# Performance work log

Measured on AMD Instinct MI355X. Metric: run time of the kernel, lower is better.

The kernel has to match this reference:

```python
import jax, jax.numpy as jnp
import numpy as np

N = 50000   # nodes per graph
E = 400000  # edges per graph (avg degree 8)
L = 16      # regex token length per edge
V = 64      # VOCAB_SIZE
EMB = 32    # REGEX_EMBEDDING_DIMENSION
H = 128     # LSTM_DIMENSION
D = 373     # hidden_vector_dim (MAX_STATES=50)
IN_IDX = 161
OUT_IDX = 320
SID = 53    # MAX_STATES + 3
SLOPE = 0.2 # GATv2 leaky_relu negative slope

def _lstm_cell(x_t, h, c, Wih, Whh, b):
    g = x_t @ Wih.T + h @ Whh.T + b          # [E, 4H], torch gate order i,f,g,o
    i, f, gg, o = jnp.split(g, 4, axis=-1)
    c = jax.nn.sigmoid(f) * c + jax.nn.sigmoid(i) * jnp.tanh(gg)
    h = jax.nn.sigmoid(o) * jnp.tanh(c)
    return h, c

def _edge_scalar(tokens, embed, Wih_f, Whh_f, b_f, Wih_r, Whh_r, b_r, W1, b1, W2, b2):
    emb = embed.at[0].set(0.0)[tokens]       # padding_idx=0; [E, L, EMB]
    En = tokens.shape[0]
    h0 = jnp.zeros((En, H), jnp.float32)
    def step(carry, x_t):
        h, c = _lstm_cell(x_t, carry[0], carry[1], Wih_f, Whh_f, b_f)
        return (h, c), None
    (h_fwd, _), _ = jax.lax.scan(step, (h0, h0), jnp.swapaxes(emb, 0, 1))
    # bidirectional output at last timestep: reverse direction has consumed only token L-1
    h_bwd, _ = _lstm_cell(emb[:, -1], h0, h0, Wih_r, Whh_r, b_r)
    feat = jax.nn.relu(jnp.concatenate([h_fwd, h_bwd], axis=-1) @ W1 + b1)
    return jax.nn.relu(feat @ W2 + b2)[:, 0]  # [E]

def _gatv2(x, src, dst, Wl, bl, Wr, br, att, bias):
    xl = x @ Wl + bl                          # source transform (messages)
    xr = x @ Wr + br                          # target transform
    m = jax.nn.leaky_relu(xl[src] + xr[dst], SLOPE)  # [E, D]
    e = m @ att                                      # [E]
    e_max = jax.ops.segment_max(e, dst, num_segments=N)
    ex = jnp.exp(e - e_max[dst])
    denom = jax.ops.segment_sum(ex, dst, num_segments=N)
    alpha = ex / (denom[dst] + 1e-16)                # scatter-softmax over in-edges
    agg = jax.ops.segment_sum(alpha[:, None] * xl[src], dst, num_segments=N)
    return agg + bias

def _process(x, ei, edge_attr, Wl, bl, Wr, br, att, bias):
    src, dst = ei[0], ei[1]
    src_id = jnp.argmax(x[src, :SID], axis=-1)
    tgt_id = jnp.argmax(x[dst, :SID], axis=-1)
    x = x.at[dst, IN_IDX + src_id].set(edge_attr)   # index_put scatter writes
    x = x.at[src, OUT_IDX + tgt_id].set(edge_attr)
    return jax.nn.relu(_gatv2(x, src, dst, Wl, bl, Wr, br, att, bias) + x)

def setup_inputs():
    key = jax.random.key(0)
    ks = jax.random.split(key, 40)
    rn = lambda k, s, sc=0.05: jax.random.normal(k, s, dtype=jnp.float32) * sc
    return {
        "fx": jax.random.normal(ks[0], (N, D), dtype=jnp.float32),
        "bx": jax.random.normal(ks[1], (N, D), dtype=jnp.float32),
        "f_edge_index": jax.random.randint(ks[2], (2, E), 0, N),
        "b_edge_index": jax.random.randint(ks[3], (2, E), 0, N),
        "f_tokens": jax.random.randint(ks[4], (E, L), 0, V),
        "b_tokens": jax.random.randint(ks[5], (E, L), 0, V),
        "embed": rn(ks[6], (V, EMB), 1.0),
        "Wih_f": rn(ks[7], (4 * H, EMB)),
        "Whh_f": rn(ks[8], (4 * H, H)),
        "bih_f": rn(ks[9], (4 * H,)),
        "bhh_f": rn(ks[10], (4 * H,)),
        "Wih_r": rn(ks[11], (4 * H, EMB)),
        "Whh_r": rn(ks[12], (4 * H, H)),
        "bih_r": rn(ks[13], (4 * H,)),
        "bhh_r": rn(ks[14], (4 * H,)),
        "W1": rn(ks[15], (2 * H, 32)),
        "b1": rn(ks[16], (32,)),
        "W2": rn(ks[17], (32, 1)),
        "b2": rn(ks[18], (1,)),
        "fWl": rn(ks[19], (D, D)), "fbl": rn(ks[20], (D,)),
        "fWr": rn(ks[21], (D, D)), "fbr": rn(ks[22], (D,)),
        "fatt": rn(ks[23], (D,)), "fbias": rn(ks[24], (D,)),
        "bWl": rn(ks[25], (D, D)), "bbl": rn(ks[26], (D,)),
        "bWr": rn(ks[27], (D, D)), "bbr": rn(ks[28], (D,)),
        "batt": rn(ks[29], (D,)), "bbias": rn(ks[30], (D,)),
    }

def reference(fx, bx, f_edge_index, b_edge_index, f_tokens, b_tokens, embed,
              Wih_f, Whh_f, bih_f, bhh_f, Wih_r, Whh_r, bih_r, bhh_r,
              W1, b1, W2, b2,
              fWl, fbl, fWr, fbr, fatt, fbias,
              bWl, bbl, bWr, bbr, batt, bbias):
    b_f = bih_f + bhh_f
    b_r = bih_r + bhh_r
    f_ea = _edge_scalar(f_tokens, embed, Wih_f, Whh_f, b_f, Wih_r, Whh_r, b_r, W1, b1, W2, b2)
    b_ea = _edge_scalar(b_tokens, embed, Wih_f, Whh_f, b_f, Wih_r, Whh_r, b_r, W1, b1, W2, b2)
    fxo = _process(fx, f_edge_index, f_ea, fWl, fbl, fWr, fbr, fatt, fbias)
    bxo = _process(bx, b_edge_index, b_ea, bWl, bbl, bWr, bbr, batt, bbias)
    return jnp.concatenate([fxo, bxo], axis=-1)  # [N, 2*D]
```

## Files before the change

### kernel.cpp

```cpp
#include <hip/hip_runtime.h>
#include <cstdint>


#define D_DIM   373
#define SID_N   53
#define IN_COL  161
#define OUT_COL 320
#define HS_STRIDE 136

typedef short bf16x8 __attribute__((ext_vector_type(8)));
typedef float f32x4  __attribute__((ext_vector_type(4)));

#define LOG2E_F 1.4426950408889634f
#define TWO_LOG2E_F 2.8853900817779268f

__device__ __forceinline__ float fast_exp2(float x) {
#if __has_builtin(__builtin_amdgcn_exp2f)
  return __builtin_amdgcn_exp2f(x);
#else
  return exp2f(x);
#endif
}
__device__ __forceinline__ float fast_rcp(float x) {
#if __has_builtin(__builtin_amdgcn_rcpf)
  return __builtin_amdgcn_rcpf(x);
#else
  return 1.0f / x;
#endif
}
__device__ __forceinline__ float sig_pre(float y)  { return fast_rcp(1.0f + fast_exp2(y)); }
__device__ __forceinline__ float tanh_pre(float y) { return 1.0f - 2.0f * fast_rcp(1.0f + fast_exp2(y)); }
__device__ __forceinline__ float tanh_pl(float x)  { return tanh_pre(TWO_LOG2E_F * x); }

__device__ __forceinline__ float sig_ref(float x)  { return 1.0f / (1.0f + __expf(-x)); }
__device__ __forceinline__ float tanh_ref(float x) { return 2.0f / (1.0f + __expf(-2.0f * x)) - 1.0f; }

__device__ __forceinline__ unsigned short f2bf(float f) {
  unsigned u = __float_as_uint(f);
  unsigned r = (u + 0x7fffu + ((u >> 16) & 1u)) >> 16;
  return (unsigned short)r;
}
__device__ __forceinline__ float bflo2f(unsigned u) { return __uint_as_float(u << 16); }
__device__ __forceinline__ float bfhi2f(unsigned u) { return __uint_as_float(u & 0xffff0000u); }
__device__ __forceinline__ unsigned cvt_pk_bf16(float lo, float hi) {
  unsigned r;
  asm("v_cvt_pk_bf16_f32 %0, %1, %2" : "=v"(r) : "v"(lo), "v"(hi));
  return r;
}

__global__ void fill_u32_kernel(unsigned* __restrict__ p, unsigned v, size_t n) {
  size_t i = (size_t)blockIdx.x * blockDim.x + threadIdx.x;
  size_t stride = (size_t)gridDim.x * blockDim.x;
  for (; i < n; i += stride) p[i] = v;
}

__global__ void precompute_kernel(
    const float* __restrict__ embed, const float* __restrict__ Wih_f,
    const float* __restrict__ Whh_f,
    const float* __restrict__ bih_f, const float* __restrict__ bhh_f,
    const float* __restrict__ Wih_r,
    const float* __restrict__ bih_r, const float* __restrict__ bhh_r,
    const float* __restrict__ W1, const float* __restrict__ b1,
    unsigned short* __restrict__ Pg, unsigned short* __restrict__ BfragW,
    unsigned short* __restrict__ Bfrag1, float* __restrict__ FB)
{
  __shared__ float ps[512];
  __shared__ float gb[512];
  __shared__ float hb[128];
  int v = blockIdx.x;
  int j = threadIdx.x;

  float s = 0.0f;
  if (v != 0) {
    #pragma unroll
    for (int k = 0; k < 32; ++k) s += embed[v * 32 + k] * Wih_f[j * 32 + k];
  }
  ps[j] = s + bih_f[j] + bhh_f[j];

  float gr = bih_r[j] + bhh_r[j];
  if (v != 0) {
    #pragma unroll
    for (int k = 0; k < 32; ++k) gr += embed[v * 32 + k] * Wih_r[j * 32 + k];
  }
  gb[j] = gr;
  __syncthreads();
  if (j < 128) {
    float c = sig_ref(gb[j]) * tanh_ref(gb[256 + j]);
    hb[j] = sig_ref(gb[384 + j]) * tanh_ref(c);
  }
  __syncthreads();

  { int h = j >> 2, g = j & 3;
    float sc = (g == 2) ? TWO_LOG2E_F : -LOG2E_F;
    Pg[((size_t)v * 128 + h) * 4 + g] = f2bf(ps[g * 128 + h] * sc); }

  if (j < 32) {
    float s2 = b1[j];
    for (int m = 0; m < 128; ++m) s2 += hb[m] * W1[(128 + m) * 32 + j];
    FB[v * 32 + j] = s2;
  }

  if (v == 0) {
    for (int f = j; f < 65536; f += 512) {
      int e = f & 7, l = (f >> 3) & 63, ks = (f >> 9) & 3, nt = f >> 11;
      int n = nt * 16 + (l & 15);
      int k = ks * 32 + (l >> 4) * 8 + e;
      float sc = ((nt >> 3) == 2) ? TWO_LOG2E_F : -LOG2E_F;
      BfragW[f] = f2bf(Whh_f[(size_t)n * 128 + k] * sc);
    }
  }
  if (v == 1) {
    for (int f = j; f < 4096; f += 512) {
      int e = f & 7, l = (f >> 3) & 63, ks = (f >> 9) & 3, n2 = f >> 11;
      int q = n2 * 16 + (l & 15);
      int k = ks * 32 + (l >> 4) * 8 + e;
      Bfrag1[f] = f2bf(W1[(size_t)k * 32 + q]);
    }
  }
}

__global__ __launch_bounds__(512, 4) void lstm_mfma_kernel(
    const int*   __restrict__ tokens,
    const unsigned short* __restrict__ Pg,
    const unsigned short* __restrict__ BfragW,
    const unsigned short* __restrict__ Bfrag1,
    const float* __restrict__ FB,
    const float* __restrict__ W2,
    const float* __restrict__ b2,
    float* __restrict__ ea, int E, int nTiles)
{
  __shared__ unsigned short Hs[2][16 * HS_STRIDE];
  __shared__ int toks[16][16];

  int tid  = threadIdx.x;
  int lane = tid & 63;
  int wv2  = tid >> 6;
  int l15  = lane & 15;
  int lg   = lane >> 4;
  int hbase = wv2 * 16 + lg * 4;

  bf16x8 BW[4][4];
  #pragma unroll
  for (int gate = 0; gate < 4; ++gate)
    #pragma unroll
    for (int ks = 0; ks < 4; ++ks)
      BW[gate][ks] = *(const bf16x8*)(BfragW +
          ((size_t)((gate * 8 + wv2) * 4 + ks) * 64 + lane) * 8);
  float4 w2lo = *(const float4*)(W2 + lg * 4);
  float4 w2hi = *(const float4*)(W2 + 16 + lg * 4);
  float b2v = b2[0];

  for (int tile = blockIdx.x; tile < nTiles; tile += gridDim.x) {
    int e0 = tile * 16;
    if (tid < 256) {
      int m = tid >> 4, t = tid & 15;
      int ee = e0 + m; if (ee >= E) ee = E - 1;
      toks[t][m] = tokens[(size_t)ee * 16 + t];
    }
    __syncthreads();

    float cst[4];
    {
      int v0 = toks[0][l15];
      const uint4* pp = (const uint4*)(Pg + ((size_t)v0 * 128 + hbase) * 4);
      uint4 pa = pp[0], pb = pp[1];
      float h[4];
      {
        float ii = sig_pre(bflo2f(pa.x)), gg = tanh_pre(bflo2f(pa.y));
        float oo = sig_pre(bfhi2f(pa.y));
        float cn = ii * gg; cst[0] = cn; h[0] = oo * tanh_pl(cn);
      }
      {
        float ii = sig_pre(bflo2f(pa.z)), gg = tanh_pre(bflo2f(pa.w));
        float oo = sig_pre(bfhi2f(pa.w));
        float cn = ii * gg; cst[1] = cn; h[1] = oo * tanh_pl(cn);
      }
      {
        float ii = sig_pre(bflo2f(pb.x)), gg = tanh_pre(bflo2f(pb.y));
        float oo = sig_pre(bfhi2f(pb.y));
        float cn = ii * gg; cst[2] = cn; h[2] = oo * tanh_pl(cn);
      }
      {
        float ii = sig_pre(bflo2f(pb.z)), gg = tanh_pre(bflo2f(pb.w));
        float oo = sig_pre(bfhi2f(pb.w));
        float cn = ii * gg; cst[3] = cn; h[3] = oo * tanh_pl(cn);
      }
      uint2 hp = make_uint2(cvt_pk_bf16(h[0], h[1]), cvt_pk_bf16(h[2], h[3]));
      *(uint2*)(&Hs[0][l15 * HS_STRIDE + hbase]) = hp;
    }
    __syncthreads();

    int cur = 0;
    #pragma unroll 1
    for (int t = 1; t < 16; ++t) {
      int vt = toks[t][l15];
      const uint4* pp = (const uint4*)(Pg + ((size_t)vt * 128 + hbase) * 4);
      uint4 pa = pp[0], pb = pp[1];
      f32x4 acc[4];
      acc[0] = (f32x4){bflo2f(pa.x), bflo2f(pa.z), bflo2f(pb.x), bflo2f(pb.z)};
      acc[1] = (f32x4){bfhi2f(pa.x), bfhi2f(pa.z), bfhi2f(pb.x), bfhi2f(pb.z)};
      acc[2] = (f32x4){bflo2f(pa.y), bflo2f(pa.w), bflo2f(pb.y), bflo2f(pb.w)};
      acc[3] = (f32x4){bfhi2f(pa.y), bfhi2f(pa.w), bfhi2f(pb.y), bfhi2f(pb.w)};

      bf16x8 Hf[4];
      #pragma unroll
      for (int ks = 0; ks < 4; ++ks)
        Hf[ks] = *(const bf16x8*)(&Hs[cur][l15 * HS_STRIDE + ks * 32 + lg * 8]);
      #pragma unroll
      for (int ks = 0; ks < 4; ++ks)
        #pragma unroll
        for (int gate = 0; gate < 4; ++gate)
          acc[gate] = __builtin_amdgcn_mfma_f32_16x16x32_bf16(
              BW[gate][ks], Hf[ks], acc[gate], 0, 0, 0);

      float h[4];
      #pragma unroll
      for (int r = 0; r < 4; ++r) {
        float ii = sig_pre(acc[0][r]);
        float ff = sig_pre(acc[1][r]);
        float gg = tanh_pre(acc[2][r]);
        float oo = sig_pre(acc[3][r]);
        float cn = fmaf(ff, cst[r], ii * gg);
        cst[r] = cn;
        h[r] = oo * tanh_pl(cn);
      }
      uint2 hp = make_uint2(cvt_pk_bf16(h[0], h[1]), cvt_pk_bf16(h[2], h[3]));
      *(uint2*)(&Hs[cur ^ 1][l15 * HS_STRIDE + hbase]) = hp;
      cur ^= 1;
      __syncthreads();
    }

    if (wv2 == 0) {
      bf16x8 Hf[4];
      #pragma unroll
      for (int ks = 0; ks < 4; ++ks)
        Hf[ks] = *(const bf16x8*)(&Hs[cur][l15 * HS_STRIDE + ks * 32 + lg * 8]);
      f32x4 a2[2];
      a2[0] = (f32x4){0.f, 0.f, 0.f, 0.f};
      a2[1] = (f32x4){0.f, 0.f, 0.f, 0.f};
      #pragma unroll
      for (int ks = 0; ks < 4; ++ks)
        #pragma unroll
        for (int n2 = 0; n2 < 2; ++n2)
          a2[n2] = __builtin_amdgcn_mfma_f32_16x16x32_bf16(
              *(const bf16x8*)(Bfrag1 + ((size_t)(n2 * 4 + ks) * 64 + lane) * 8),
              Hf[ks], a2[n2], 0, 0, 0);
      int v15 = toks[15][l15];
      float4 fb0 = *(const float4*)(FB + v15 * 32 + lg * 4);
      float4 fb1 = *(const float4*)(FB + v15 * 32 + 16 + lg * 4);
      float pr = fmaxf(a2[0][0] + fb0.x, 0.f) * w2lo.x
               + fmaxf(a2[0][1] + fb0.y, 0.f) * w2lo.y
               + fmaxf(a2[0][2] + fb0.z, 0.f) * w2lo.z
               + fmaxf(a2[0][3] + fb0.w, 0.f) * w2lo.w
               + fmaxf(a2[1][0] + fb1.x, 0.f) * w2hi.x
               + fmaxf(a2[1][1] + fb1.y, 0.f) * w2hi.y
               + fmaxf(a2[1][2] + fb1.z, 0.f) * w2hi.z
               + fmaxf(a2[1][3] + fb1.w, 0.f) * w2hi.w;
      pr += __shfl_xor(pr, 16);
      pr += __shfl_xor(pr, 32);
      int eidx = e0 + l15;
      if (lane < 16 && eidx < E) ea[eidx] = fmaxf(pr + b2v, 0.0f);
    }
    __syncthreads();
  }
}

__global__ void argmax_winner_kernel(
    const float* __restrict__ x, const int* __restrict__ ei, int E,
    int* __restrict__ srcid, int* __restrict__ tgtid,
    int* __restrict__ win_in, int* __restrict__ win_out)
{
  int e = blockIdx.x * 256 + threadIdx.x;
  if (e >= E) return;
  int s = ei[e];
  int t = ei[E + e];
  const float* xs = x + (size_t)s * D_DIM;
  int sid = 0; float bv = xs[0];
  for (int k = 1; k < SID_N; ++k) { float v = xs[k]; if (v > bv) { bv = v; sid = k; } }
  const float* xt = x + (size_t)t * D_DIM;
  int tix = 0; bv = xt[0];
  for (int k = 1; k < SID_N; ++k) { float v = xt[k]; if (v > bv) { bv = v; tix = k; } }
  srcid[e] = sid;
  tgtid[e] = tix;
  atomicMax(&win_in[(size_t)t * SID_N + sid], e);
  atomicMax(&win_out[(size_t)s * SID_N + tix], e);
}

__global__ void scatter_resolve_kernel(
    const int* __restrict__ ei, const float* __restrict__ ea,
    const int* __restrict__ srcid, const int* __restrict__ tgtid,
    const int* __restrict__ win_in, const int* __restrict__ win_out,
    float* __restrict__ x_mod, int E)
{
  int e = blockIdx.x * 256 + threadIdx.x;
  if (e >= E) return;
  int s = ei[e];
  int t = ei[E + e];
  int sid = srcid[e], tix = tgtid[e];
  if (win_in[(size_t)t * SID_N + sid] == e)
    x_mod[(size_t)t * D_DIM + IN_COL + sid] = ea[e];
  if (win_out[(size_t)s * SID_N + tix] == e)
    x_mod[(size_t)s * D_DIM + OUT_COL + tix] = ea[e];
}

__global__ void pack_w_kernel(const float* __restrict__ Wl,
                              const float* __restrict__ Wr,
                              unsigned short* __restrict__ Wfrag)
{
  int f = blockIdx.x * 256 + threadIdx.x;
  if (f >= 48 * 12 * 64 * 8) return;
  int e = f & 7, l = (f >> 3) & 63;
  int rest = f >> 9;
  int ks = rest % 12, nt = rest / 12;
  int nl = nt * 16 + (l & 15);
  int k  = ks * 32 + (l >> 4) * 8 + e;
  float val = 0.0f;
  if (k < D_DIM) {
    if (nl < D_DIM)                      val = Wl[(size_t)k * D_DIM + nl];
    else if (nl >= 384 && nl < 384 + D_DIM) val = Wr[(size_t)k * D_DIM + (nl - 384)];
  }
  Wfrag[f] = f2bf(val);
}

__global__ __launch_bounds__(256, 2) void gemm_mfma_kernel(
    const float* __restrict__ A,
    const unsigned short* __restrict__ Wfrag,
    const float* __restrict__ bl, const float* __restrict__ br,
    float* __restrict__ xl, float* __restrict__ xr, int N)
{
  __shared__ unsigned short As[64][40];
  int tid  = threadIdx.x;
  int lane = tid & 63;
  int wv   = tid >> 6;
  int l15  = lane & 15, lg = lane >> 4;
  int m0   = blockIdx.x * 64;
  int nt   = blockIdx.y * 4 + wv;

  f32x4 acc[4];
  #pragma unroll
  for (int i = 0; i < 4; ++i) acc[i] = (f32x4){0.f, 0.f, 0.f, 0.f};

  int srow = tid >> 2, seg = tid & 3;
  int gr = m0 + srow; if (gr >= N) gr = N - 1;
  const float* arow = A + (size_t)gr * D_DIM;

  for (int ks = 0; ks < 12; ++ks) {
    int c0 = ks * 32 + seg * 8;
    float v[8];
    #pragma unroll
    for (int j = 0; j < 8; ++j) v[j] = (c0 + j < D_DIM) ? arow[c0 + j] : 0.0f;
    unsigned pk0 = cvt_pk_bf16(v[0], v[1]);
    unsigned pk1 = cvt_pk_bf16(v[2], v[3]);
    unsigned pk2 = cvt_pk_bf16(v[4], v[5]);
    unsigned pk3 = cvt_pk_bf16(v[6], v[7]);
    __syncthreads();
    *(uint4*)(&As[srow][seg * 8]) = make_uint4(pk0, pk1, pk2, pk3);
    __syncthreads();

    bf16x8 Bf = *(const bf16x8*)(Wfrag + ((size_t)(nt * 12 + ks) * 64 + lane) * 8);
    #pragma unroll
    for (int msub = 0; msub < 4; ++msub) {
      bf16x8 Af = *(const bf16x8*)(&As[msub * 16 + l15][lg * 8]);
      acc[msub] = __builtin_amdgcn_mfma_f32_16x16x32_bf16(Af, Bf, acc[msub], 0, 0, 0);
    }
  }

  int nl = nt * 16 + l15;
  float* dst = nullptr; int col = 0; const float* bias_ = nullptr;
  if (nl < D_DIM)                         { dst = xl; col = nl;       bias_ = bl; }
  else if (nl >= 384 && nl < 384 + D_DIM) { dst = xr; col = nl - 384; bias_ = br; }
  if (dst) {
    float bv = bias_[col];
    #pragma unroll
    for (int msub = 0; msub < 4; ++msub) {
      #pragma unroll
      for (int r = 0; r < 4; ++r) {
        int m = m0 + msub * 16 + lg * 4 + r;
        if (m < N) dst[(size_t)m * D_DIM + col] = acc[msub][r] + bv;
      }
    }
  }
}

__global__ __launch_bounds__(256) void edge_e_kernel(
    const float* __restrict__ xl, const float* __restrict__ xr,
    const float* __restrict__ att, const int* __restrict__ ei,
    float* __restrict__ e_buf, int E)
{
  int widx = (blockIdx.x * 256 + threadIdx.x) >> 6;
  int lane = threadIdx.x & 63;
  if (widx >= E) return;
  int s = ei[widx], t = ei[E + widx];
  const float* pl = xl + (size_t)s * D_DIM;
  const float* pr = xr + (size_t)t * D_DIM;
  float acc = 0.0f;
  for (int d = lane; d < D_DIM; d += 64) {
    float m = pl[d] + pr[d];
    m = (m > 0.0f) ? m : 0.2f * m;
    acc += m * att[d];
  }
  #pragma unroll
  for (int o = 32; o > 0; o >>= 1) acc += __shfl_down(acc, o);
  if (lane == 0) e_buf[widx] = acc;
}

__global__ void hist_kernel(const int* __restrict__ ei, unsigned* __restrict__ deg,
                            int E) {
  int e = blockIdx.x * 256 + threadIdx.x;
  if (e >= E) return;
  atomicAdd(&deg[ei[E + e]], 1u);
}

__global__ void scan1_kernel(const unsigned* __restrict__ deg,
                             unsigned* __restrict__ excl,
                             unsigned* __restrict__ bsum, int n) {
  __shared__ unsigned s[256];
  int t = threadIdx.x;
  int i = blockIdx.x * 256 + t;
  unsigned v = (i < n) ? deg[i] : 0u;
  s[t] = v; __syncthreads();
  #pragma unroll
  for (int o = 1; o < 256; o <<= 1) {
    unsigned u = (t >= o) ? s[t - o] : 0u;
    __syncthreads();
    s[t] += u;
    __syncthreads();
  }
  if (i < n) excl[i] = s[t] - v;
  if (t == 255) bsum[blockIdx.x] = s[255];
}

__global__ void scan2_kernel(unsigned* __restrict__ bsum, int nb) {
  __shared__ unsigned s[256];
  int t = threadIdx.x;
  unsigned v = (t < nb) ? bsum[t] : 0u;
  s[t] = v; __syncthreads();
  #pragma unroll
  for (int o = 1; o < 256; o <<= 1) {
    unsigned u = (t >= o) ? s[t - o] : 0u;
    __syncthreads();
    s[t] += u;
    __syncthreads();
  }
  if (t < nb) bsum[t] = s[t] - v;
}

__global__ void scan3_kernel(unsigned* __restrict__ excl,
                             const unsigned* __restrict__ bsum, int n) {
  int i = blockIdx.x * 256 + threadIdx.x;
  if (i < n) excl[i] += bsum[i >> 8];
}

__global__ void place_kernel(const int* __restrict__ ei,
                             unsigned* __restrict__ offs,
                             int* __restrict__ csr_eid, int E) {
  int e = blockIdx.x * 256 + threadIdx.x;
  if (e >= E) return;
  unsigned j = atomicAdd(&offs[ei[E + e]], 1u);
  csr_eid[j] = e;
}

__global__ __launch_bounds__(256) void node_gat_kernel(
    const int* __restrict__ ei, const int* __restrict__ csr_eid,
    const unsigned* __restrict__ offs, const unsigned* __restrict__ deg,
    const float* __restrict__ ebuf, const float* __restrict__ xl,
    const float* __restrict__ xmod, const float* __restrict__ bias,
    float* __restrict__ out, int N, int E, int goff)
{
  int n = (blockIdx.x * 256 + threadIdx.x) >> 6;
  int lane = threadIdx.x & 63;
  if (n >= N) return;
  unsigned end = offs[n], d = deg[n], start = end - d;

  float mx = -3.4e38f;
  for (unsigned j = start; j < end; ++j)
    mx = fmaxf(mx, ebuf[csr_eid[j]]);
  float den = 0.0f;
  for (unsigned j = start; j < end; ++j)
    den += __expf(ebuf[csr_eid[j]] - mx);
  float inv = 1.0f / (den + 1e-16f);

  float o0 = 0, o1 = 0, o2 = 0, o3 = 0, o4 = 0, o5 = 0;
  for (unsigned j = start; j < end; ++j) {
    int eid = csr_eid[j];
    float w = __expf(ebuf[eid] - mx) * inv;
    const float* row = xl + (size_t)ei[eid] * D_DIM;
    o0 = fmaf(w, row[lane], o0);
    o1 = fmaf(w, row[64 + lane], o1);
    o2 = fmaf(w, row[128 + lane], o2);
    o3 = fmaf(w, row[192 + lane], o3);
    o4 = fmaf(w, row[256 + lane], o4);
    if (lane < 53) o5 = fmaf(w, row[320 + lane], o5);
  }

  const float* xm = xmod + (size_t)n * D_DIM;
  float* op = out + (size_t)n * (2 * D_DIM) + goff;
  op[lane]       = fmaxf(o0 + bias[lane]       + xm[lane],       0.0f);
  op[64 + lane]  = fmaxf(o1 + bias[64 + lane]  + xm[64 + lane],  0.0f);
  op[128 + lane] = fmaxf(o2 + bias[128 + lane] + xm[128 + lane], 0.0f);
  op[192 + lane] = fmaxf(o3 + bias[192 + lane] + xm[192 + lane], 0.0f);
  op[256 + lane] = fmaxf(o4 + bias[256 + lane] + xm[256 + lane], 0.0f);
  if (lane < 53)
    op[320 + lane] = fmaxf(o5 + bias[320 + lane] + xm[320 + lane], 0.0f);
}

extern "C" void kernel_launch(void* const* d_in, const int* in_sizes, int n_in,
                              void* d_out, int out_size, void* d_ws, size_t ws_size,
                              hipStream_t stream)
{
  const float* fx     = (const float*)d_in[0];
  const float* bx     = (const float*)d_in[1];
  const int*   fei    = (const int*)d_in[2];
  const int*   bei    = (const int*)d_in[3];
  const int*   ftk    = (const int*)d_in[4];
  const int*   btk    = (const int*)d_in[5];
  const float* embed  = (const float*)d_in[6];
  const float* Wih_f  = (const float*)d_in[7];
  const float* Whh_f  = (const float*)d_in[8];
  const float* bih_f  = (const float*)d_in[9];
  const float* bhh_f  = (const float*)d_in[10];
  const float* Wih_r  = (const float*)d_in[11];
  const float* bih_r  = (const float*)d_in[13];
  const float* bhh_r  = (const float*)d_in[14];
  const float* W1     = (const float*)d_in[15];
  const float* b1     = (const float*)d_in[16];
  const float* W2     = (const float*)d_in[17];
  const float* b2     = (const float*)d_in[18];

  const float* Wl_g[2]   = {(const float*)d_in[19], (const float*)d_in[25]};
  const float* bl_g[2]   = {(const float*)d_in[20], (const float*)d_in[26]};
  const float* Wr_g[2]   = {(const float*)d_in[21], (const float*)d_in[27]};
  const float* br_g[2]   = {(const float*)d_in[22], (const float*)d_in[28]};
  const float* att_g[2]  = {(const float*)d_in[23], (const float*)d_in[29]};
  const float* bias_g[2] = {(const float*)d_in[24], (const float*)d_in[30]};
  const float* x_g[2]    = {fx, bx};
  const int*   ei_g[2]   = {fei, bei};
  const int*   tk_g[2]   = {ftk, btk};

  const int E = in_sizes[2] / 2;
  const int N = in_sizes[0] / D_DIM;
  (void)att_g;

  char* wsb = (char*)d_ws;
  size_t off = 0;
  auto alloc = [&](size_t bytes) -> void* {
    void* p = wsb + off; off += (bytes + 255) & ~(size_t)255; return p;
  };
  unsigned short* Pg     = (unsigned short*)alloc((size_t)64 * 128 * 4 * 2);
  unsigned short* BfragW = (unsigned short*)alloc((size_t)65536 * 2);
  unsigned short* Bfrag1 = (unsigned short*)alloc((size_t)4096 * 2);
  unsigned short* Wfrag2 = (unsigned short*)alloc((size_t)2 * 294912 * 2);
  float* FB    = (float*)alloc((size_t)64 * 32 * 4);
  float* ea    = (float*)alloc((size_t)E * 4);
  float* ebuf  = (float*)alloc((size_t)E * 4);
  int*   srcid = (int*)alloc((size_t)E * 4);
  int*   tgtid = (int*)alloc((size_t)E * 4);
  int*   csr_eid = (int*)alloc((size_t)E * 4);
  unsigned* deg  = (unsigned*)alloc((size_t)N * 4);
  unsigned* offs = (unsigned*)alloc((size_t)N * 4);
  unsigned* bsum = (unsigned*)alloc((size_t)256 * 4);
  int* win_in  = (int*)alloc((size_t)N * SID_N * 4);
  int* win_out = (int*)alloc((size_t)N * SID_N * 4);
  float* xmod  = (float*)alloc((size_t)N * D_DIM * 4);
  float* xl    = (float*)alloc((size_t)N * D_DIM * 4);
  float* xr    = (float*)alloc((size_t)N * D_DIM * 4);
  (void)ws_size; (void)n_in; (void)out_size;

  const size_t win_u32 = (size_t)((char*)win_out - (char*)win_in) / 4
                         + (size_t)N * SID_N;

  float* out = (float*)d_out;

  precompute_kernel<<<64, 512, 0, stream>>>(
      embed, Wih_f, Whh_f, bih_f, bhh_f, Wih_r, bih_r, bhh_r, W1, b1,
      Pg, BfragW, Bfrag1, FB);
  pack_w_kernel<<<(294912 + 255) / 256, 256, 0, stream>>>(
      Wl_g[0], Wr_g[0], Wfrag2);
  pack_w_kernel<<<(294912 + 255) / 256, 256, 0, stream>>>(
      Wl_g[1], Wr_g[1], Wfrag2 + 294912);

  const int nTiles  = (E + 15) / 16;
  const int gridL   = nTiles < 2048 ? nTiles : 2048;
  const int gridE   = (E + 255) / 256;
  const int gridEW  = (E + 3) / 4;
  const int nScanB  = (N + 255) / 256;
  const int gridNd  = (N * 64 + 255) / 256;
  dim3 gridG((N + 63) / 64, 12);

  for (int g = 0; g < 2; ++g) {
    const float* x  = x_g[g];
    const int*   ei = ei_g[g];

    lstm_mfma_kernel<<<gridL, 512, 0, stream>>>(tk_g[g], Pg, BfragW, Bfrag1,
                                                FB, W2, b2, ea, E, nTiles);

    hipMemcpyAsync(xmod, x, (size_t)N * D_DIM * sizeof(float),
                   hipMemcpyDeviceToDevice, stream);
    fill_u32_kernel<<<2048, 256, 0, stream>>>((unsigned*)win_in, 0xFFFFFFFFu,
                                              win_u32);
    argmax_winner_kernel<<<gridE, 256, 0, stream>>>(x, ei, E, srcid, tgtid,
                                                    win_in, win_out);
    scatter_resolve_kernel<<<gridE, 256, 0, stream>>>(ei, ea, srcid, tgtid,
                                                      win_in, win_out, xmod, E);

    gemm_mfma_kernel<<<gridG, 256, 0, stream>>>(xmod, Wfrag2 + (size_t)g * 294912,
                                                bl_g[g], br_g[g], xl, xr, N);

    fill_u32_kernel<<<512, 256, 0, stream>>>(deg, 0u, (size_t)N);
    hist_kernel<<<gridE, 256, 0, stream>>>(ei, deg, E);
    scan1_kernel<<<nScanB, 256, 0, stream>>>(deg, offs, bsum, N);
    scan2_kernel<<<1, 256, 0, stream>>>(bsum, nScanB);
    scan3_kernel<<<nScanB, 256, 0, stream>>>(offs, bsum, N);
    place_kernel<<<gridE, 256, 0, stream>>>(ei, offs, csr_eid, E);

    edge_e_kernel<<<gridEW, 256, 0, stream>>>(xl, xr, att_g[g], ei, ebuf, E);
    node_gat_kernel<<<gridNd, 256, 0, stream>>>(ei, csr_eid, offs, deg, ebuf,
                                                xl, xmod, bias_g[g], out,
                                                N, E, g * D_DIM);
  }
}
```

Before: 3.986 ms.

## Process 64 edges per LSTM tile, merge sigmoid-tanh reciprocals, cache softmax exps

Each LSTM block now handles 64 edges per tile instead of 16. Each wave runs four 16-edge sub-tiles per timestep, which cuts the number of barriers per edge and reuses the register-held recurrent weights across more work. The gate activations are rewritten so that sigmoid(i)*tanh(g) and sigmoid(o)*tanh(c) each need one reciprocal instead of two. The GAT node kernel stores the exponentials back into ebuf so the aggregation pass does not recompute them. The trade-offs are more shared memory and registers per block, which may lower occupancy, possible overflow in the fused reciprocal form for large exponents, and the GAT kernel now writing to ebuf.

```diff
diff --git a/kernel.cpp b/kernel.cpp
--- a/kernel.cpp
+++ b/kernel.cpp
@@ -7,6 +7,7 @@
 #define IN_COL  161
 #define OUT_COL 320
 #define HS_STRIDE 136
+#define EDGES_T 64
 
 typedef short bf16x8 __attribute__((ext_vector_type(8)));
 typedef float f32x4  __attribute__((ext_vector_type(4)));
@@ -28,10 +29,6 @@
   return 1.0f / x;
 #endif
 }
-__device__ __forceinline__ float sig_pre(float y)  { return fast_rcp(1.0f + fast_exp2(y)); }
-__device__ __forceinline__ float tanh_pre(float y) { return 1.0f - 2.0f * fast_rcp(1.0f + fast_exp2(y)); }
-__device__ __forceinline__ float tanh_pl(float x)  { return tanh_pre(TWO_LOG2E_F * x); }
-
 __device__ __forceinline__ float sig_ref(float x)  { return 1.0f / (1.0f + __expf(-x)); }
 __device__ __forceinline__ float tanh_ref(float x) { return 2.0f / (1.0f + __expf(-2.0f * x)) - 1.0f; }
 
@@ -46,6 +43,9 @@
   unsigned r;
   asm("v_cvt_pk_bf16_f32 %0, %1, %2" : "=v"(r) : "v"(lo), "v"(hi));
   return r;
+}
+__device__ __forceinline__ float pair_sig_tanh(float A, float B) {
+  return (B - 1.0f) * fast_rcp((1.0f + A) * (1.0f + B));
 }
 
 __global__ void fill_u32_kernel(unsigned* __restrict__ p, unsigned v, size_t n) {
@@ -129,8 +129,8 @@
     const float* __restrict__ b2,
     float* __restrict__ ea, int E, int nTiles)
 {
-  __shared__ unsigned short Hs[2][16 * HS_STRIDE];
-  __shared__ int toks[16][16];
+  __shared__ unsigned short Hs[2][EDGES_T * HS_STRIDE];
+  __shared__ int toks[16][EDGES_T];
 
   int tid  = threadIdx.x;
   int lane = tid & 63;
@@ -151,90 +151,91 @@
   float b2v = b2[0];
 
   for (int tile = blockIdx.x; tile < nTiles; tile += gridDim.x) {
-    int e0 = tile * 16;
-    if (tid < 256) {
-      int m = tid >> 4, t = tid & 15;
+    int e0 = tile * EDGES_T;
+    for (int i = tid; i < 16 * EDGES_T; i += 512) {
+      int m = i >> 4, t = i & 15;
       int ee = e0 + m; if (ee >= E) ee = E - 1;
       toks[t][m] = tokens[(size_t)ee * 16 + t];
     }
     __syncthreads();
 
-    float cst[4];
-    {
-      int v0 = toks[0][l15];
+    f32x4 cst[4];
+    #pragma unroll
+    for (int es = 0; es < 4; ++es) {
+      int eL = es * 16 + l15;
+      int v0 = toks[0][eL];
       const uint4* pp = (const uint4*)(Pg + ((size_t)v0 * 128 + hbase) * 4);
       uint4 pa = pp[0], pb = pp[1];
+      float pi[4] = {bflo2f(pa.x), bflo2f(pa.z), bflo2f(pb.x), bflo2f(pb.z)};
+      float pg[4] = {bflo2f(pa.y), bflo2f(pa.w), bflo2f(pb.y), bflo2f(pb.w)};
+      float po[4] = {bfhi2f(pa.y), bfhi2f(pa.w), bfhi2f(pb.y), bfhi2f(pb.w)};
       float h[4];
-      {
-        float ii = sig_pre(bflo2f(pa.x)), gg = tanh_pre(bflo2f(pa.y));
-        float oo = sig_pre(bfhi2f(pa.y));
-        float cn = ii * gg; cst[0] = cn; h[0] = oo * tanh_pl(cn);
-      }
-      {
-        float ii = sig_pre(bflo2f(pa.z)), gg = tanh_pre(bflo2f(pa.w));
-        float oo = sig_pre(bfhi2f(pa.w));
-        float cn = ii * gg; cst[1] = cn; h[1] = oo * tanh_pl(cn);
-      }
-      {
-        float ii = sig_pre(bflo2f(pb.x)), gg = tanh_pre(bflo2f(pb.y));
-        float oo = sig_pre(bfhi2f(pb.y));
-        float cn = ii * gg; cst[2] = cn; h[2] = oo * tanh_pl(cn);
-      }
-      {
-        float ii = sig_pre(bflo2f(pb.z)), gg = tanh_pre(bflo2f(pb.w));
-        float oo = sig_pre(bfhi2f(pb.w));
-        float cn = ii * gg; cst[3] = cn; h[3] = oo * tanh_pl(cn);
+      #pragma unroll
+      for (int r = 0; r < 4; ++r) {
+        float A = fast_exp2(pi[r]);
+        float B = fast_exp2(pg[r]);
+        float O = fast_exp2(po[r]);
+        float cn = pair_sig_tanh(A, B);
+        cst[es][r] = cn;
+        float C = fast_exp2(TWO_LOG2E_F * cn);
+        h[r] = pair_sig_tanh(O, C);
       }
       uint2 hp = make_uint2(cvt_pk_bf16(h[0], h[1]), cvt_pk_bf16(h[2], h[3]));
-      *(uint2*)(&Hs[0][l15 * HS_STRIDE + hbase]) = hp;
+      *(uint2*)(&Hs[0][eL * HS_STRIDE + hbase]) = hp;
     }
     __syncthreads();
 
     int cur = 0;
     #pragma unroll 1
     for (int t = 1; t < 16; ++t) {
-      int vt = toks[t][l15];
-      const uint4* pp = (const uint4*)(Pg + ((size_t)vt * 128 + hbase) * 4);
-      uint4 pa = pp[0], pb = pp[1];
-      f32x4 acc[4];
-      acc[0] = (f32x4){bflo2f(pa.x), bflo2f(pa.z), bflo2f(pb.x), bflo2f(pb.z)};
-      acc[1] = (f32x4){bfhi2f(pa.x), bfhi2f(pa.z), bfhi2f(pb.x), bfhi2f(pb.z)};
-      acc[2] = (f32x4){bflo2f(pa.y), bflo2f(pa.w), bflo2f(pb.y), bflo2f(pb.w)};
-      acc[3] = (f32x4){bfhi2f(pa.y), bfhi2f(pa.w), bfhi2f(pb.y), bfhi2f(pb.w)};
-
+      #pragma unroll
+      for (int es = 0; es < 4; ++es) {
+        int eL = es * 16 + l15;
+        int vt = toks[t][eL];
+        const uint4* pp = (const uint4*)(Pg + ((size_t)vt * 128 + hbase) * 4);
+        uint4 pa = pp[0], pb = pp[1];
+        f32x4 acc[4];
+        acc[0] = (f32x4){bflo2f(pa.x), bflo2f(pa.z), bflo2f(pb.x), bflo2f(pb.z)};
+        acc[1] = (f32x4){bfhi2f(pa.x), bfhi2f(pa.z), bfhi2f(pb.x), bfhi2f(pb.z)};
+        acc[2] = (f32x4){bflo2f(pa.y), bflo2f(pa.w), bflo2f(pb.y), bflo2f(pb.w)};
+        acc[3] = (f32x4){bfhi2f(pa.y), bfhi2f(pa.w), bfhi2f(pb.y), bfhi2f(pb.w)};
+
+        #pragma unroll
+        for (int ks = 0; ks < 4; ++ks) {
+          bf16x8 Hf = *(const bf16x8*)(&Hs[cur][eL * HS_STRIDE + ks * 32 + lg * 8]);
+          #pragma unroll
+          for (int gate = 0; gate < 4; ++gate)
+            acc[gate] = __builtin_amdgcn_mfma_f32_16x16x32_bf16(
+                BW[gate][ks], Hf, acc[gate], 0, 0, 0);
+        }
+
+        float h[4];
+        #pragma unroll
+        for (int r = 0; r < 4; ++r) {
+          float A = fast_exp2(acc[0][r]);
+          float F = fast_exp2(acc[1][r]);
+          float B = fast_exp2(acc[2][r]);
+          float O = fast_exp2(acc[3][r]);
+          float ig = pair_sig_tanh(A, B);
+          float f  = fast_rcp(1.0f + F);
+          float cn = fmaf(f, cst[es][r], ig);
+          cst[es][r] = cn;
+          float C = fast_exp2(TWO_LOG2E_F * cn);
+          h[r] = pair_sig_tanh(O, C);
+        }
+        uint2 hp = make_uint2(cvt_pk_bf16(h[0], h[1]), cvt_pk_bf16(h[2], h[3]));
+        *(uint2*)(&Hs[cur ^ 1][eL * HS_STRIDE + hbase]) = hp;
+      }
+      cur ^= 1;
+      __syncthreads();
+    }
+
+    if (wv2 < 4) {
+      int eL = wv2 * 16 + l15;
       bf16x8 Hf[4];
       #pragma unroll
       for (int ks = 0; ks < 4; ++ks)
-        Hf[ks] = *(const bf16x8*)(&Hs[cur][l15 * HS_STRIDE + ks * 32 + lg * 8]);
-      #pragma unroll
-      for (int ks = 0; ks < 4; ++ks)
-        #pragma unroll
-        for (int gate = 0; gate < 4; ++gate)
-          acc[gate] = __builtin_amdgcn_mfma_f32_16x16x32_bf16(
-              BW[gate][ks], Hf[ks], acc[gate], 0, 0, 0);
-
-      float h[4];
-      #pragma unroll
-      for (int r = 0; r < 4; ++r) {
-        float ii = sig_pre(acc[0][r]);
-        float ff = sig_pre(acc[1][r]);
-        float gg = tanh_pre(acc[2][r]);
-        float oo = sig_pre(acc[3][r]);
-        float cn = fmaf(ff, cst[r], ii * gg);
-        cst[r] = cn;
-        h[r] = oo * tanh_pl(cn);
-      }
-      uint2 hp = make_uint2(cvt_pk_bf16(h[0], h[1]), cvt_pk_bf16(h[2], h[3]));
-      *(uint2*)(&Hs[cur ^ 1][l15 * HS_STRIDE + hbase]) = hp;
-      cur ^= 1;
-      __syncthreads();
-    }
-
-    if (wv2 == 0) {
-      bf16x8 Hf[4];
-      #pragma unroll
-      for (int ks = 0; ks < 4; ++ks)
-        Hf[ks] = *(const bf16x8*)(&Hs[cur][l15 * HS_STRIDE + ks * 32 + lg * 8]);
+        Hf[ks] = *(const bf16x8*)(&Hs[cur][eL * HS_STRIDE + ks * 32 + lg * 8]);
       f32x4 a2[2];
       a2[0] = (f32x4){0.f, 0.f, 0.f, 0.f};
       a2[1] = (f32x4){0.f, 0.f, 0.f, 0.f};
@@ -245,7 +246,7 @@
           a2[n2] = __builtin_amdgcn_mfma_f32_16x16x32_bf16(
               *(const bf16x8*)(Bfrag1 + ((size_t)(n2 * 4 + ks) * 64 + lane) * 8),
               Hf[ks], a2[n2], 0, 0, 0);
-      int v15 = toks[15][l15];
+      int v15 = toks[15][eL];
       float4 fb0 = *(const float4*)(FB + v15 * 32 + lg * 4);
       float4 fb1 = *(const float4*)(FB + v15 * 32 + 16 + lg * 4);
       float pr = fmaxf(a2[0][0] + fb0.x, 0.f) * w2lo.x
@@ -258,7 +259,7 @@
                + fmaxf(a2[1][3] + fb1.w, 0.f) * w2hi.w;
       pr += __shfl_xor(pr, 16);
       pr += __shfl_xor(pr, 32);
-      int eidx = e0 + l15;
+      int eidx = e0 + eL;
       if (lane < 16 && eidx < E) ea[eidx] = fmaxf(pr + b2v, 0.0f);
     }
     __syncthreads();
@@ -463,7 +464,7 @@
 __global__ __launch_bounds__(256) void node_gat_kernel(
     const int* __restrict__ ei, const int* __restrict__ csr_eid,
     const unsigned* __restrict__ offs, const unsigned* __restrict__ deg,
-    const float* __restrict__ ebuf, const float* __restrict__ xl,
+    float* __restrict__ ebuf, const float* __restrict__ xl,
     const float* __restrict__ xmod, const float* __restrict__ bias,
     float* __restrict__ out, int N, int E, int goff)
 {
@@ -476,14 +477,18 @@
   for (unsigned j = start; j < end; ++j)
     mx = fmaxf(mx, ebuf[csr_eid[j]]);
   float den = 0.0f;
-  for (unsigned j = start; j < end; ++j)
-    den += __expf(ebuf[csr_eid[j]] - mx);
+  for (unsigned j = start; j < end; ++j) {
+    int eid = csr_eid[j];
+    float ex = __expf(ebuf[eid] - mx);
+    ebuf[eid] = ex;
+    den += ex;
+  }
   float inv = 1.0f / (den + 1e-16f);
 
   float o0 = 0, o1 = 0, o2 = 0, o3 = 0, o4 = 0, o5 = 0;
   for (unsigned j = start; j < end; ++j) {
     int eid = csr_eid[j];
-    float w = __expf(ebuf[eid] - mx) * inv;
+    float w = ebuf[eid] * inv;
     const float* row = xl + (size_t)ei[eid] * D_DIM;
     o0 = fmaf(w, row[lane], o0);
     o1 = fmaf(w, row[64 + lane], o1);
@@ -539,7 +544,6 @@
 
   const int E = in_sizes[2] / 2;
   const int N = in_sizes[0] / D_DIM;
-  (void)att_g;
 
   char* wsb = (char*)d_ws;
   size_t off = 0;
@@ -579,7 +583,7 @@
   pack_w_kernel<<<(294912 + 255) / 256, 256, 0, stream>>>(
       Wl_g[1], Wr_g[1], Wfrag2 + 294912);
 
-  const int nTiles  = (E + 15) / 16;
+  const int nTiles  = (E + EDGES_T - 1) / EDGES_T;
   const int gridL   = nTiles < 2048 ? nTiles : 2048;
   const int gridE   = (E + 255) / 256;
   const int gridEW  = (E + 3) / 4;
```

Result: faster. 3.614 ms (-9.3%).
